# Kernel optimization log

Hardware: AMD Instinct MI355X
Metric: run time of the kernel (lower is better)

Reference implementation:

```python
import jax, jax.numpy as jnp
import numpy as np

B = 2
D_MODEL = 256
D_FFN = 1024
N_LEVELS = 4
N_HEADS = 8
N_POINTS = 4
D_HEAD = D_MODEL // N_HEADS
SHAPES = np.array([[128, 128], [64, 64], [32, 32], [16, 16]], dtype=np.int32)  # (H, W) per level
LEN = int(SHAPES.prod(axis=1).sum())  # 21760
EPS = 1e-5


def _layer_norm(x, g, b):
    m = jnp.mean(x, axis=-1, keepdims=True)
    v = jnp.mean(jnp.square(x - m), axis=-1, keepdims=True)
    return (x - m) * jax.lax.rsqrt(v + EPS) * g + b


def _bilinear_gather(v_l, loc, H, W):
    # v_l: [B, H*W, NH, DH]; loc: [B, L, NH, NP, 2] in normalized [0,1] coords (x, y)
    # grid_sample(align_corners=False, padding_mode=zeros) semantics: pixel = loc * size - 0.5
    x = loc[..., 0] * W - 0.5
    y = loc[..., 1] * H - 0.5
    x0 = jnp.floor(x)
    y0 = jnp.floor(y)
    dx = x - x0
    dy = y - y0
    x0i = x0.astype(jnp.int32)
    y0i = y0.astype(jnp.int32)
    b_ix = jnp.arange(v_l.shape[0])[:, None, None, None]
    h_ix = jnp.arange(v_l.shape[2])[None, None, :, None]

    def corner(xi, yi, w):
        valid = (xi >= 0) & (xi < W) & (yi >= 0) & (yi < H)
        idx = jnp.clip(yi, 0, H - 1) * W + jnp.clip(xi, 0, W - 1)
        v = v_l[b_ix, idx, h_ix]  # [B, L, NH, NP, DH]
        return v * (w * valid.astype(v.dtype))[..., None]

    return (corner(x0i, y0i, (1 - dx) * (1 - dy))
            + corner(x0i + 1, y0i, dx * (1 - dy))
            + corner(x0i, y0i + 1, (1 - dx) * dy)
            + corner(x0i + 1, y0i + 1, dx * dy))


def _forward(src, pos, reference_points,
             w_off, b_off, w_attn, b_attn, w_val, b_val, w_out, b_out,
             ln1_g, ln1_b, w1, b1, w2, b2, ln2_g, ln2_b,
             spatial_shapes, level_start_index, padding_mask):
    shapes = np.asarray(spatial_shapes)        # static per-level (H, W)
    starts = np.asarray(level_start_index)     # static level offsets
    Bsz, L, _ = src.shape

    # ---- MSDeformAttn ----
    q = src + pos                              # with_pos_embed
    value = src @ w_val + b_val
    value = jnp.where(padding_mask[..., None], 0.0, value)
    value = value.reshape(Bsz, L, N_HEADS, D_HEAD)

    off = (q @ w_off + b_off).reshape(Bsz, L, N_HEADS, N_LEVELS, N_POINTS, 2)
    attn = (q @ w_attn + b_attn).reshape(Bsz, L, N_HEADS, N_LEVELS * N_POINTS)
    attn = jax.nn.softmax(attn, axis=-1).reshape(Bsz, L, N_HEADS, N_LEVELS, N_POINTS)

    wh = jnp.asarray(shapes[:, ::-1].copy(), dtype=src.dtype)  # [NL, 2] = (W, H)
    loc = reference_points[:, :, None, :, None, :] + off / wh[None, None, None, :, None, :]

    out = jnp.zeros((Bsz, L, N_HEADS, D_HEAD), src.dtype)
    for l in range(N_LEVELS):
        H, W = int(shapes[l, 0]), int(shapes[l, 1])
        s = int(starts[l])
        v_l = value[:, s:s + H * W]                          # [B, H*W, NH, DH]
        sampled = _bilinear_gather(v_l, loc[:, :, :, l], H, W)  # [B, L, NH, NP, DH]
        out = out + (sampled * attn[:, :, :, l][..., None]).sum(axis=3)
    attn_out = out.reshape(Bsz, L, D_MODEL) @ w_out + b_out

    # ---- residual + LN + FFN + residual + LN (dropout = identity in eval) ----
    x = _layer_norm(src + attn_out, ln1_g, ln1_b)
    ffn = jax.nn.relu(x @ w1 + b1) @ w2 + b2
    return _layer_norm(x + ffn, ln2_g, ln2_b)


def setup_inputs() -> dict:
    key = jax.random.key(0)
    ks = jax.random.split(key, 16)
    s = 0.02
    n_off = N_HEADS * N_LEVELS * N_POINTS
    level_start = np.concatenate([[0], SHAPES.prod(axis=1).cumsum()[:-1]]).astype(np.int32)
    return {
        "src": jax.random.normal(ks[0], (B, LEN, D_MODEL), jnp.float32),
        "pos": jax.random.normal(ks[1], (B, LEN, D_MODEL), jnp.float32),
        "reference_points": jax.random.uniform(ks[2], (B, LEN, N_LEVELS, 2), jnp.float32),
        "spatial_shapes": jnp.asarray(SHAPES),
        "level_start_index": jnp.asarray(level_start),
        "padding_mask": jnp.zeros((B, LEN), jnp.bool_),
        "w_off": jax.random.normal(ks[3], (D_MODEL, n_off * 2), jnp.float32) * s,
        "b_off": jax.random.normal(ks[4], (n_off * 2,), jnp.float32) * 0.5,
        "w_attn": jax.random.normal(ks[5], (D_MODEL, n_off), jnp.float32) * s,
        "b_attn": jnp.zeros((n_off,), jnp.float32),
        "w_val": jax.random.normal(ks[6], (D_MODEL, D_MODEL), jnp.float32) * s,
        "b_val": jnp.zeros((D_MODEL,), jnp.float32),
        "w_out": jax.random.normal(ks[7], (D_MODEL, D_MODEL), jnp.float32) * s,
        "b_out": jnp.zeros((D_MODEL,), jnp.float32),
        "ln1_g": jnp.ones((D_MODEL,), jnp.float32),
        "ln1_b": jnp.zeros((D_MODEL,), jnp.float32),
        "w1": jax.random.normal(ks[8], (D_MODEL, D_FFN), jnp.float32) * s,
        "b1": jnp.zeros((D_FFN,), jnp.float32),
        "w2": jax.random.normal(ks[9], (D_FFN, D_MODEL), jnp.float32) * s,
        "b2": jnp.zeros((D_MODEL,), jnp.float32),
        "ln2_g": jnp.ones((D_MODEL,), jnp.float32),
        "ln2_b": jnp.zeros((D_MODEL,), jnp.float32),
    }


def reference(src, pos, reference_points, spatial_shapes, level_start_index, padding_mask,
              w_off, b_off, w_attn, b_attn, w_val, b_val, w_out, b_out,
              ln1_g, ln1_b, w1, b1, w2, b2, ln2_g, ln2_b):
    return _forward(src, pos, reference_points,
                    w_off, b_off, w_attn, b_attn, w_val, b_val, w_out, b_out,
                    ln1_g, ln1_b, w1, b1, w2, b2, ln2_g, ln2_b,
                    spatial_shapes, level_start_index, padding_mask)
```

## Files before the change

kernel.cpp:

```cpp
#include <hip/hip_runtime.h>
#include <hip/hip_bf16.h>

#define BSZ      2
#define LTOK     21760
#define NTOK     (BSZ * LTOK)
#define DMODEL   256
#define DFFN     1024

typedef __attribute__((ext_vector_type(8))) short short8;
typedef __attribute__((ext_vector_type(4))) float f32x4;

__device__ __forceinline__ unsigned short f2bf(float x) {
    __hip_bfloat16 h = __float2bfloat16(x);
    return *reinterpret_cast<unsigned short*>(&h);
}
__device__ __forceinline__ float bf2f(unsigned short u) {
    union { unsigned int i; float f; } c; c.i = ((unsigned int)u) << 16; return c.f;
}
__device__ __forceinline__ float bflo(unsigned int u) {
    union { unsigned int i; float f; } c; c.i = u << 16; return c.f;
}
__device__ __forceinline__ float bfhi(unsigned int u) {
    union { unsigned int i; float f; } c; c.i = u & 0xffff0000u; return c.f;
}

#define TM 128
#define TN 128
#define TBK 32

__global__ __launch_bounds__(256) void gemm_mfma(
    const void* __restrict__ Av, const float* __restrict__ A2,
    const unsigned short* __restrict__ Bt, const float* __restrict__ bias,
    float* __restrict__ Cf, unsigned short* __restrict__ Cb,
    int M, int N, int K, int amode, int relu, int cmode,
    const unsigned char* __restrict__ mask)
{
    __shared__ __align__(16) unsigned short sA[TM * TBK];
    __shared__ __align__(16) unsigned short sB[TN * TBK];

    const int tid  = threadIdx.x;
    const int lane = tid & 63;
    const int wave = tid >> 6;
    const int wm = wave >> 1, wn = wave & 1;

    const int bm = blockIdx.y * TM;
    const int bn = blockIdx.x * TN;

    const int sr = tid >> 6;
    const int fr = lane & 15;
    const int fk = (lane >> 4) * 8;

    f32x4 acc[4][4];
    #pragma unroll
    for (int i = 0; i < 4; ++i)
        #pragma unroll
        for (int j = 0; j < 4; ++j)
            acc[i][j] = (f32x4){0.f, 0.f, 0.f, 0.f};

    for (int k0 = 0; k0 < K; k0 += TBK) {
        #pragma unroll
        for (int rr = 0; rr < 2; ++rr) {
            const int s = sr + rr * 4;
            const size_t grow = (size_t)(bm + s * 16 + fr);
            unsigned short* dst = &sA[s * 512 + lane * 8];
            if (amode == 0) {
                const float* Af = (const float*)Av + grow * K + k0 + fk;
                float4 v0 = *(const float4*)Af;
                float4 v1 = *(const float4*)(Af + 4);
                if (A2) {
                    const float* Pf = A2 + grow * K + k0 + fk;
                    const float4 p0 = *(const float4*)Pf;
                    const float4 p1 = *(const float4*)(Pf + 4);
                    v0.x += p0.x; v0.y += p0.y; v0.z += p0.z; v0.w += p0.w;
                    v1.x += p1.x; v1.y += p1.y; v1.z += p1.z; v1.w += p1.w;
                }
                const unsigned int p0 = (unsigned)f2bf(v0.x) | ((unsigned)f2bf(v0.y) << 16);
                const unsigned int p1 = (unsigned)f2bf(v0.z) | ((unsigned)f2bf(v0.w) << 16);
                const unsigned int p2 = (unsigned)f2bf(v1.x) | ((unsigned)f2bf(v1.y) << 16);
                const unsigned int p3 = (unsigned)f2bf(v1.z) | ((unsigned)f2bf(v1.w) << 16);
                *(uint4*)dst = make_uint4(p0, p1, p2, p3);
            } else {
                const unsigned short* Ab = (const unsigned short*)Av + grow * K + k0 + fk;
                *(uint4*)dst = *(const uint4*)Ab;
            }
        }
        #pragma unroll
        for (int rr = 0; rr < 2; ++rr) {
            const int s = sr + rr * 4;
            const size_t gn = (size_t)(bn + s * 16 + fr);
            *(uint4*)&sB[s * 512 + lane * 8] = *(const uint4*)(Bt + gn * K + k0 + fk);
        }
        __syncthreads();

        short8 af[4], bfr[4];
        #pragma unroll
        for (int i = 0; i < 4; ++i)
            af[i] = *(const short8*)&sA[(wm * 4 + i) * 512 + lane * 8];
        #pragma unroll
        for (int j = 0; j < 4; ++j)
            bfr[j] = *(const short8*)&sB[(wn * 4 + j) * 512 + lane * 8];
        #pragma unroll
        for (int i = 0; i < 4; ++i)
            #pragma unroll
            for (int j = 0; j < 4; ++j)
                acc[i][j] = __builtin_amdgcn_mfma_f32_16x16x32_bf16(
                    af[i], bfr[j], acc[i][j], 0, 0, 0);
        __syncthreads();
    }

    const int r0 = (lane >> 4) * 4;
    const int c0 = lane & 15;
    #pragma unroll
    for (int j = 0; j < 4; ++j) {
        const int col = bn + wn * 64 + j * 16 + c0;
        const float bj = bias ? bias[col] : 0.f;
        #pragma unroll
        for (int i = 0; i < 4; ++i) {
            #pragma unroll
            for (int r = 0; r < 4; ++r) {
                const int row = bm + wm * 64 + i * 16 + r0 + r;
                float v = acc[i][j][r] + bj;
                if (relu) v = fmaxf(v, 0.f);
                if (mask && mask[row]) v = 0.f;
                if (cmode == 1) {
                    const int bb = row >= LTOK;
                    const int srow = row - bb * LTOK;
                    const int h = col >> 5, d = col & 31;
                    Cb[((size_t)(bb * 8 + h) * LTOK + srow) * 32 + d] = f2bf(v);
                } else {
                    if (Cf) Cf[(size_t)row * N + col] = v;
                    if (Cb) Cb[(size_t)row * N + col] = f2bf(v);
                }
            }
        }
    }
}

__global__ void transpose_cast(const float* __restrict__ W,
                               unsigned short* __restrict__ Wt, int K, int N)
{
    __shared__ float t[32][33];
    const int k0 = blockIdx.x * 32, n0 = blockIdx.y * 32;
    const int tx = threadIdx.x, ty = threadIdx.y;
    #pragma unroll
    for (int i = 0; i < 32; i += 8)
        t[ty + i][tx] = W[(size_t)(k0 + ty + i) * N + n0 + tx];
    __syncthreads();
    #pragma unroll
    for (int i = 0; i < 32; i += 8)
        Wt[(size_t)(n0 + ty + i) * K + k0 + tx] = f2bf(t[tx][ty + i]);
}

__global__ void concat_bias(const float* __restrict__ b_off,
                            const float* __restrict__ b_att,
                            float* __restrict__ dst)
{
    const int t = threadIdx.x;
    dst[t] = (t < 256) ? b_off[t] : b_att[t - 256];
}

__global__ __launch_bounds__(256) void sample_kernel(
    const unsigned short* __restrict__ vT, const float* __restrict__ qp,
    const float* __restrict__ ref,
    const int* __restrict__ sshapes, const int* __restrict__ lstart,
    unsigned short* __restrict__ samp)
{
    __shared__ float s_w[256][4];
    __shared__ int   s_o[256][4];

    const int blk   = blockIdx.x;
    const int plane = blk & 15;
    const int chunk = blk >> 4;
    const int b = plane >> 3;
    const int h = plane & 7;
    const int s0 = chunk * 16;
    const int t = threadIdx.x;

    {
        const int tl = t >> 4;
        const int p  = t & 15;
        const int l  = p >> 2;
        const int pp = p & 3;
        const int H = sshapes[2 * l], W = sshapes[2 * l + 1];
        const float Wf = (float)W, Hf = (float)H;
        const size_t tok = (size_t)(b * LTOK + s0 + tl);

        const float ox = qp[tok * 384 + h * 32 + l * 8 + pp * 2 + 0];
        const float oy = qp[tok * 384 + h * 32 + l * 8 + pp * 2 + 1];
        const float rx = ref[tok * 8 + l * 2 + 0];
        const float ry = ref[tok * 8 + l * 2 + 1];

        const float x = (rx + ox / Wf) * Wf - 0.5f;
        const float y = (ry + oy / Hf) * Hf - 0.5f;
        const float x0 = floorf(x), y0 = floorf(y);
        const float dx = x - x0, dy = y - y0;
        const int x0i = (int)x0, y0i = (int)y0;
        const int s = lstart[l];

        const float a = qp[tok * 384 + 256 + h * 16 + p];
        float mx = a;
        #pragma unroll
        for (int m = 8; m; m >>= 1) mx = fmaxf(mx, __shfl_xor(mx, m, 16));
        const float e = __expf(a - mx);
        float ssum = e;
        #pragma unroll
        for (int m = 8; m; m >>= 1) ssum += __shfl_xor(ssum, m, 16);
        const float prob = e / ssum;

        const float cw[4] = {(1.f - dx) * (1.f - dy), dx * (1.f - dy),
                             (1.f - dx) * dy,         dx * dy};
        const int cx[4] = {x0i, x0i + 1, x0i,     x0i + 1};
        const int cy[4] = {y0i, y0i,     y0i + 1, y0i + 1};
        #pragma unroll
        for (int c = 0; c < 4; ++c) {
            const bool valid = (cx[c] >= 0) & (cx[c] < W) & (cy[c] >= 0) & (cy[c] < H);
            const int xi = min(max(cx[c], 0), W - 1);
            const int yi = min(max(cy[c], 0), H - 1);
            s_o[t][c] = (s + yi * W + xi) * 64;
            s_w[t][c] = valid ? cw[c] * prob : 0.f;
        }
    }
    __syncthreads();

    const int tl = t >> 4;
    const int dp = t & 15;
    const char* vp = (const char*)(vT + (size_t)plane * LTOK * 32) + dp * 4;
    float acc0 = 0.f, acc1 = 0.f;
    #pragma unroll
    for (int p = 0; p < 16; ++p) {
        const int sl = tl * 16 + p;
        #pragma unroll
        for (int c = 0; c < 4; ++c) {
            const float w = s_w[sl][c];
            const unsigned int u = *(const unsigned int*)(vp + s_o[sl][c]);
            acc0 = fmaf(w, bflo(u), acc0);
            acc1 = fmaf(w, bfhi(u), acc1);
        }
    }
    const unsigned int o = (unsigned)f2bf(acc0) | ((unsigned)f2bf(acc1) << 16);
    *(unsigned int*)(samp + (size_t)(b * LTOK + s0 + tl) * 256 + h * 32 + dp * 2) = o;
}

__global__ __launch_bounds__(256) void ln_kernel(
    const void* __restrict__ a, int a_bf16,
    const void* __restrict__ b, int b_bf16,
    const float* __restrict__ g, const float* __restrict__ be,
    float* __restrict__ outF, unsigned short* __restrict__ outB)
{
    const int wid  = threadIdx.x >> 6;
    const int lane = threadIdx.x & 63;
    const int tok  = blockIdx.x * 4 + wid;
    const size_t base = (size_t)tok * 256 + lane * 4;

    float4 va, vb;
    if (a_bf16) {
        const ushort4 u = *(const ushort4*)((const unsigned short*)a + base);
        va.x = bf2f(u.x); va.y = bf2f(u.y); va.z = bf2f(u.z); va.w = bf2f(u.w);
    } else {
        va = *(const float4*)((const float*)a + base);
    }
    if (b_bf16) {
        const ushort4 u = *(const ushort4*)((const unsigned short*)b + base);
        vb.x = bf2f(u.x); vb.y = bf2f(u.y); vb.z = bf2f(u.z); vb.w = bf2f(u.w);
    } else {
        vb = *(const float4*)((const float*)b + base);
    }
    float4 v;
    v.x = va.x + vb.x; v.y = va.y + vb.y; v.z = va.z + vb.z; v.w = va.w + vb.w;

    float s  = v.x + v.y + v.z + v.w;
    float sq = v.x * v.x + v.y * v.y + v.z * v.z + v.w * v.w;
    #pragma unroll
    for (int m = 32; m; m >>= 1) {
        s  += __shfl_xor(s, m, 64);
        sq += __shfl_xor(sq, m, 64);
    }
    const float mean = s * (1.f / 256.f);
    const float var  = sq * (1.f / 256.f) - mean * mean;
    const float rs   = rsqrtf(var + 1e-5f);

    const float4 g4 = *(const float4*)(g + lane * 4);
    const float4 b4 = *(const float4*)(be + lane * 4);
    float4 o;
    o.x = (v.x - mean) * rs * g4.x + b4.x;
    o.y = (v.y - mean) * rs * g4.y + b4.y;
    o.z = (v.z - mean) * rs * g4.z + b4.z;
    o.w = (v.w - mean) * rs * g4.w + b4.w;
    if (outF) *(float4*)(outF + base) = o;
    if (outB) {
        ushort4 u;
        u.x = f2bf(o.x); u.y = f2bf(o.y); u.z = f2bf(o.z); u.w = f2bf(o.w);
        *(ushort4*)(outB + base) = u;
    }
}

extern "C" void kernel_launch(void* const* d_in, const int* in_sizes, int n_in,
                              void* d_out, int out_size, void* d_ws, size_t ws_size,
                              hipStream_t stream)
{
    const float* src   = (const float*)d_in[0];
    const float* pos   = (const float*)d_in[1];
    const float* ref   = (const float*)d_in[2];
    const int*   sshap = (const int*)d_in[3];
    const int*   lstrt = (const int*)d_in[4];
    const unsigned char* mask = (const unsigned char*)d_in[5];
    const float* w_off = (const float*)d_in[6];
    const float* b_off = (const float*)d_in[7];
    const float* w_att = (const float*)d_in[8];
    const float* b_att = (const float*)d_in[9];
    const float* w_val = (const float*)d_in[10];
    const float* b_val = (const float*)d_in[11];
    const float* w_out = (const float*)d_in[12];
    const float* b_out = (const float*)d_in[13];
    const float* ln1g  = (const float*)d_in[14];
    const float* ln1b  = (const float*)d_in[15];
    const float* w1    = (const float*)d_in[16];
    const float* b1    = (const float*)d_in[17];
    const float* w2    = (const float*)d_in[18];
    const float* b2    = (const float*)d_in[19];
    const float* ln2g  = (const float*)d_in[20];
    const float* ln2b  = (const float*)d_in[21];
    float* out = (float*)d_out;

    const size_t SZB = (size_t)NTOK * 256 * 4;
    char* w = (char*)d_ws;
    float*          qpf    = (float*)w;
    float*          aof    = (float*)w;
    unsigned short* hidb   = (unsigned short*)w;
    unsigned short* vT     = (unsigned short*)(w + SZB * 3 / 2);
    unsigned short* samp16 = (unsigned short*)(w + SZB * 2);
    unsigned short* ffb    = samp16;
    unsigned short* xb     = (unsigned short*)(w + SZB * 2 + SZB / 2);
    char* wreg = w + SZB * 3;
    unsigned short* wvalT  = (unsigned short*)wreg;
    unsigned short* woaT   = wvalT + 256 * 256;
    unsigned short* woutT  = woaT + 384 * 256;
    unsigned short* w1T    = woutT + 256 * 256;
    unsigned short* w2T    = w1T + 1024 * 256;
    float*          bcat   = (float*)(w2T + 256 * 1024);

    const dim3 blk(256);
    const dim3 tblk(32, 8);

    transpose_cast<<<dim3(8, 8),  tblk, 0, stream>>>(w_val, wvalT, 256, 256);
    transpose_cast<<<dim3(8, 8),  tblk, 0, stream>>>(w_off, woaT,  256, 256);
    transpose_cast<<<dim3(8, 4),  tblk, 0, stream>>>(w_att, woaT + 256 * 256, 256, 128);
    transpose_cast<<<dim3(8, 8),  tblk, 0, stream>>>(w_out, woutT, 256, 256);
    transpose_cast<<<dim3(8, 32), tblk, 0, stream>>>(w1,    w1T,   256, 1024);
    transpose_cast<<<dim3(32, 8), tblk, 0, stream>>>(w2,    w2T,   1024, 256);
    concat_bias<<<1, 384, 0, stream>>>(b_off, b_att, bcat);

    gemm_mfma<<<dim3(2, NTOK / TM), blk, 0, stream>>>(
        src, nullptr, wvalT, b_val, nullptr, vT, NTOK, 256, 256, 0, 0, 1, mask);
    gemm_mfma<<<dim3(3, NTOK / TM), blk, 0, stream>>>(
        src, pos, woaT, bcat, qpf, nullptr, NTOK, 384, 256, 0, 0, 0, nullptr);

    sample_kernel<<<dim3(16 * (LTOK / 16)), blk, 0, stream>>>(
        vT, qpf, ref, sshap, lstrt, samp16);

    gemm_mfma<<<dim3(2, NTOK / TM), blk, 0, stream>>>(
        samp16, nullptr, woutT, b_out, aof, nullptr, NTOK, 256, 256, 1, 0, 0, nullptr);

    ln_kernel<<<dim3(NTOK / 4), blk, 0, stream>>>(
        src, 0, aof, 0, ln1g, ln1b, nullptr, xb);

    gemm_mfma<<<dim3(8, NTOK / TM), blk, 0, stream>>>(
        xb, nullptr, w1T, b1, nullptr, hidb, NTOK, DFFN, 256, 1, 1, 0, nullptr);
    gemm_mfma<<<dim3(2, NTOK / TM), blk, 0, stream>>>(
        hidb, nullptr, w2T, b2, nullptr, ffb, NTOK, 256, DFFN, 1, 0, 0, nullptr);

    ln_kernel<<<dim3(NTOK / 4), blk, 0, stream>>>(
        xb, 1, ffb, 1, ln2g, ln2b, out, nullptr);
}
```

Before: 547.6 us.

## Stage GEMM epilogue through LDS for vectorized bf16 stores; store qp and attn-out in bf16

The GEMM epilogue now writes each 16-row slab of accumulators as bf16 into a padded shared-memory buffer, then writes it out as 16-byte coalesced stores, including the head-major layout used for the value tensor. The float32 output path is removed, so the offset/attention projection and the output projection now write bf16, and the sampling and layernorm kernels read bf16. This cuts global store traffic and replaces scattered 2-byte stores with wide ones. The cost is extra barriers in the epilogue and lower precision for sampling offsets and attention logits, which could affect accuracy.

```diff
diff --git a/kernel.cpp b/kernel.cpp
--- a/kernel.cpp
+++ b/kernel.cpp
@@ -27,16 +27,18 @@
 #define TM 128
 #define TN 128
 #define TBK 32
+#define EBS 132
 
 __global__ __launch_bounds__(256) void gemm_mfma(
     const void* __restrict__ Av, const float* __restrict__ A2,
     const unsigned short* __restrict__ Bt, const float* __restrict__ bias,
-    float* __restrict__ Cf, unsigned short* __restrict__ Cb,
+    unsigned short* __restrict__ Cb,
     int M, int N, int K, int amode, int relu, int cmode,
     const unsigned char* __restrict__ mask)
 {
-    __shared__ __align__(16) unsigned short sA[TM * TBK];
-    __shared__ __align__(16) unsigned short sB[TN * TBK];
+    __shared__ __align__(16) unsigned short smem[TM * TBK + TN * TBK];
+    unsigned short* sA = smem;
+    unsigned short* sB = smem + TM * TBK;
 
     const int tid  = threadIdx.x;
     const int lane = tid & 63;
@@ -110,27 +112,40 @@
 
     const int r0 = (lane >> 4) * 4;
     const int c0 = lane & 15;
-    #pragma unroll
-    for (int j = 0; j < 4; ++j) {
-        const int col = bn + wn * 64 + j * 16 + c0;
-        const float bj = bias ? bias[col] : 0.f;
-        #pragma unroll
-        for (int i = 0; i < 4; ++i) {
+    unsigned short* eb = smem;
+
+    #pragma unroll
+    for (int i = 0; i < 4; ++i) {
+        if (i) __syncthreads();
+        #pragma unroll
+        for (int j = 0; j < 4; ++j) {
+            const int col = bn + wn * 64 + j * 16 + c0;
+            const float bj = bias ? bias[col] : 0.f;
             #pragma unroll
             for (int r = 0; r < 4; ++r) {
                 const int row = bm + wm * 64 + i * 16 + r0 + r;
                 float v = acc[i][j][r] + bj;
                 if (relu) v = fmaxf(v, 0.f);
                 if (mask && mask[row]) v = 0.f;
-                if (cmode == 1) {
-                    const int bb = row >= LTOK;
-                    const int srow = row - bb * LTOK;
-                    const int h = col >> 5, d = col & 31;
-                    Cb[((size_t)(bb * 8 + h) * LTOK + srow) * 32 + d] = f2bf(v);
-                } else {
-                    if (Cf) Cf[(size_t)row * N + col] = v;
-                    if (Cb) Cb[(size_t)row * N + col] = f2bf(v);
-                }
+                eb[(wm * 16 + r0 + r) * EBS + wn * 64 + j * 16 + c0] = f2bf(v);
+            }
+        }
+        __syncthreads();
+        #pragma unroll
+        for (int qq = 0; qq < 2; ++qq) {
+            const int q  = tid + qq * 256;
+            const int rl = q >> 4;
+            const int ch = q & 15;
+            const int grow = bm + (rl >> 4) * 64 + i * 16 + (rl & 15);
+            const uint4 val = *(const uint4*)&eb[rl * EBS + ch * 8];
+            if (cmode == 1) {
+                const int bb   = grow >= LTOK;
+                const int srow = grow - bb * LTOK;
+                const int hcol = (bn + ch * 8) >> 5;
+                const int d    = (ch & 3) * 8;
+                *(uint4*)&Cb[((size_t)(bb * 8 + hcol) * LTOK + srow) * 32 + d] = val;
+            } else {
+                *(uint4*)&Cb[(size_t)grow * N + bn + ch * 8] = val;
             }
         }
     }
@@ -160,7 +175,7 @@
 }
 
 __global__ __launch_bounds__(256) void sample_kernel(
-    const unsigned short* __restrict__ vT, const float* __restrict__ qp,
+    const unsigned short* __restrict__ vT, const unsigned short* __restrict__ qp,
     const float* __restrict__ ref,
     const int* __restrict__ sshapes, const int* __restrict__ lstart,
     unsigned short* __restrict__ samp)
@@ -185,8 +200,8 @@
         const float Wf = (float)W, Hf = (float)H;
         const size_t tok = (size_t)(b * LTOK + s0 + tl);
 
-        const float ox = qp[tok * 384 + h * 32 + l * 8 + pp * 2 + 0];
-        const float oy = qp[tok * 384 + h * 32 + l * 8 + pp * 2 + 1];
+        const float ox = bf2f(qp[tok * 384 + h * 32 + l * 8 + pp * 2 + 0]);
+        const float oy = bf2f(qp[tok * 384 + h * 32 + l * 8 + pp * 2 + 1]);
         const float rx = ref[tok * 8 + l * 2 + 0];
         const float ry = ref[tok * 8 + l * 2 + 1];
 
@@ -197,7 +212,7 @@
         const int x0i = (int)x0, y0i = (int)y0;
         const int s = lstart[l];
 
-        const float a = qp[tok * 384 + 256 + h * 16 + p];
+        const float a = bf2f(qp[tok * 384 + 256 + h * 16 + p]);
         float mx = a;
         #pragma unroll
         for (int m = 8; m; m >>= 1) mx = fmaxf(mx, __shfl_xor(mx, m, 16));
@@ -324,8 +339,8 @@
 
     const size_t SZB = (size_t)NTOK * 256 * 4;
     char* w = (char*)d_ws;
-    float*          qpf    = (float*)w;
-    float*          aof    = (float*)w;
+    unsigned short* qpb    = (unsigned short*)w;
+    unsigned short* aof16  = (unsigned short*)w;
     unsigned short* hidb   = (unsigned short*)w;
     unsigned short* vT     = (unsigned short*)(w + SZB * 3 / 2);
     unsigned short* samp16 = (unsigned short*)(w + SZB * 2);
@@ -351,23 +366,23 @@
     concat_bias<<<1, 384, 0, stream>>>(b_off, b_att, bcat);
 
     gemm_mfma<<<dim3(2, NTOK / TM), blk, 0, stream>>>(
-        src, nullptr, wvalT, b_val, nullptr, vT, NTOK, 256, 256, 0, 0, 1, mask);
+        src, nullptr, wvalT, b_val, vT, NTOK, 256, 256, 0, 0, 1, mask);
     gemm_mfma<<<dim3(3, NTOK / TM), blk, 0, stream>>>(
-        src, pos, woaT, bcat, qpf, nullptr, NTOK, 384, 256, 0, 0, 0, nullptr);
+        src, pos, woaT, bcat, qpb, NTOK, 384, 256, 0, 0, 0, nullptr);
 
     sample_kernel<<<dim3(16 * (LTOK / 16)), blk, 0, stream>>>(
-        vT, qpf, ref, sshap, lstrt, samp16);
+        vT, qpb, ref, sshap, lstrt, samp16);
 
     gemm_mfma<<<dim3(2, NTOK / TM), blk, 0, stream>>>(
-        samp16, nullptr, woutT, b_out, aof, nullptr, NTOK, 256, 256, 1, 0, 0, nullptr);
+        samp16, nullptr, woutT, b_out, aof16, NTOK, 256, 256, 1, 0, 0, nullptr);
 
     ln_kernel<<<dim3(NTOK / 4), blk, 0, stream>>>(
-        src, 0, aof, 0, ln1g, ln1b, nullptr, xb);
+        src, 0, aof16, 1, ln1g, ln1b, nullptr, xb);
 
     gemm_mfma<<<dim3(8, NTOK / TM), blk, 0, stream>>>(
-        xb, nullptr, w1T, b1, nullptr, hidb, NTOK, DFFN, 256, 1, 1, 0, nullptr);
+        xb, nullptr, w1T, b1, hidb, NTOK, DFFN, 256, 1, 1, 0, nullptr);
     gemm_mfma<<<dim3(2, NTOK / TM), blk, 0, stream>>>(
-        hidb, nullptr, w2T, b2, nullptr, ffb, NTOK, 256, DFFN, 1, 0, 0, nullptr);
+        hidb, nullptr, w2T, b2, ffb, NTOK, 256, DFFN, 1, 0, 0, nullptr);
 
     ln_kernel<<<dim3(NTOK / 4), blk, 0, stream>>>(
         xb, 1, ffb, 1, ln2g, ln2b, out, nullptr);
```

After: 522.9 us. 1.05x faster.
